# Kernel optimization log

Measured on AMD Instinct MI355X. Metric: run time of the kernel, lower is better.

Reference implementation:

```python
import jax, jax.numpy as jnp
import numpy as np

C_M, C_Z, C, N_HEAD = 256, 128, 32, 8
N_SEQ, N_RES = 256, 256
LN_EPS = 1e-5


def _layer_norm(x, w, b):
    mu = jnp.mean(x, axis=-1, keepdims=True)
    var = jnp.var(x, axis=-1, keepdims=True)
    return (x - mu) * jax.lax.rsqrt(var + LN_EPS) * w + b


def setup_inputs() -> dict:
    key = jax.random.key(0)
    ks = jax.random.split(key, 12)
    s = 0.02
    return {
        "m": jax.random.normal(ks[0], (N_SEQ, N_RES, C_M), dtype=jnp.float32),
        "z": jax.random.normal(ks[1], (N_RES, N_RES, C_Z), dtype=jnp.float32),
        "ln_m_w": jnp.ones((C_M,), jnp.float32),
        "ln_m_b": jnp.zeros((C_M,), jnp.float32),
        "ln_z_w": jnp.ones((C_Z,), jnp.float32),
        "ln_z_b": jnp.zeros((C_Z,), jnp.float32),
        "Wz": jax.random.normal(ks[2], (C_Z, N_HEAD), dtype=jnp.float32) * s,
        "Wq": jax.random.normal(ks[3], (C_M, N_HEAD * C), dtype=jnp.float32) * s,
        "Wk": jax.random.normal(ks[4], (C_M, N_HEAD * C), dtype=jnp.float32) * s,
        "Wv": jax.random.normal(ks[5], (C_M, N_HEAD * C), dtype=jnp.float32) * s,
        "Wg": jax.random.normal(ks[6], (C_M, N_HEAD * C), dtype=jnp.float32) * s,
        "bg": jnp.zeros((N_HEAD * C,), jnp.float32),
        "Wo": jax.random.normal(ks[7], (N_HEAD * C, C_M), dtype=jnp.float32) * s,
        "bo": jnp.zeros((C_M,), jnp.float32),
    }


def reference(m, z, ln_m_w, ln_m_b, ln_z_w, ln_z_b, Wz, Wq, Wk, Wv, Wg, bg, Wo, bo):
    S, R, cm = m.shape
    mn = _layer_norm(m, ln_m_w, ln_m_b)            # (S, R, c_m)
    zn = _layer_norm(z, ln_z_w, ln_z_b)            # (R, R, c_z)
    bias = jnp.einsum('qkz,zh->hqk', zn, Wz)       # (H, R, R), pair bias per head

    Wqh = Wq.reshape(cm, N_HEAD, C)
    Wkh = Wk.reshape(cm, N_HEAD, C)
    Wvh = Wv.reshape(cm, N_HEAD, C)
    q = jnp.einsum('srm,mhc->shrc', mn, Wqh)       # (S, H, R, c)
    k = jnp.einsum('srm,mhc->shrc', mn, Wkh)
    v = jnp.einsum('srm,mhc->shrc', mn, Wvh)

    scale = 1.0 / jnp.sqrt(jnp.asarray(C, mn.dtype))
    scores = jnp.einsum('shqc,shkc->shqk', q, k) * scale + bias[None]  # (S, H, R, R)
    attn = jax.nn.softmax(scores, axis=-1)
    o = jnp.einsum('shqk,shkc->shqc', attn, v)     # (S, H, R, c)
    o = o.transpose(0, 2, 1, 3).reshape(S, R, N_HEAD * C)

    g = jax.nn.sigmoid(mn @ Wg + bg)               # gating, (S, R, H*c)
    return (g * o) @ Wo + bo                       # (S, R, c_m)
```

## Files before the change

kernel.cpp:

```cpp
#include <hip/hip_runtime.h>
#include <cmath>

#define NSEQ 256
#define NRES 256
#define CM   256
#define CZ   128
#define NHEAD 8
#define CHD  32
#define NROW 65536

typedef __attribute__((ext_vector_type(8))) short short8;
typedef __attribute__((ext_vector_type(4))) short s16x4;
typedef __attribute__((ext_vector_type(4))) float f32x4;

__device__ __forceinline__ unsigned short f2bf(float x) {
    union { float f; unsigned int u; } v; v.f = x;
    unsigned int u = v.u;
    u += 0x7fffu + ((u >> 16) & 1u);
    return (unsigned short)(u >> 16);
}
__device__ __forceinline__ float bf2f(unsigned short b) {
    union { float f; unsigned int u; } v; v.u = ((unsigned int)b) << 16;
    return v.f;
}

__device__ __forceinline__ void async16(const void* g, void* l) {
    __builtin_amdgcn_global_load_lds(
        (const __attribute__((address_space(1))) unsigned int*)g,
        (__attribute__((address_space(3))) unsigned int*)l, 16, 0, 0);
}

__device__ __forceinline__ void xcd_remap(int& x, int& y) {
    const int nx = gridDim.x, ny = gridDim.y;
    const int b = blockIdx.x + blockIdx.y * nx;
    if ((ny & 7) == 0) {
        const int c = b & 7;
        const int t = b >> 3;
        x = t % nx;
        y = c + 8 * (t / nx);
    } else {
        x = blockIdx.x; y = blockIdx.y;
    }
}

__global__ void __launch_bounds__(64)
ln_m_kernel(const float* __restrict__ m, const float* __restrict__ w,
            const float* __restrict__ b, unsigned short* __restrict__ mbf) {
    const int row = blockIdx.x;
    const int t = threadIdx.x;
    const float* x = m + (size_t)row * CM;
    float4 xv = *(const float4*)(x + t * 4);
    float s  = xv.x + xv.y + xv.z + xv.w;
    float s2 = xv.x * xv.x + xv.y * xv.y + xv.z * xv.z + xv.w * xv.w;
#pragma unroll
    for (int off = 32; off > 0; off >>= 1) {
        s  += __shfl_xor(s, off);
        s2 += __shfl_xor(s2, off);
    }
    const float mu  = s * (1.0f / CM);
    const float var = s2 * (1.0f / CM) - mu * mu;
    const float inv = rsqrtf(var + 1e-5f);
    float4 wv = *(const float4*)(w + t * 4);
    float4 bv = *(const float4*)(b + t * 4);
    ushort4 o4;
    o4.x = f2bf((xv.x - mu) * inv * wv.x + bv.x);
    o4.y = f2bf((xv.y - mu) * inv * wv.y + bv.y);
    o4.z = f2bf((xv.z - mu) * inv * wv.z + bv.z);
    o4.w = f2bf((xv.w - mu) * inv * wv.w + bv.w);
    *(ushort4*)(mbf + (size_t)row * CM + t * 4) = o4;
}

__global__ void __launch_bounds__(64)
ln_z_bias_kernel(const float* __restrict__ z, const float* __restrict__ w,
                 const float* __restrict__ b, const float* __restrict__ Wz,
                 float* __restrict__ bias) {
    const int pair = blockIdx.x;
    const int t = threadIdx.x;
    const float* x = z + (size_t)pair * CZ;
    float2 xv = *(const float2*)(x + t * 2);
    float s  = xv.x + xv.y;
    float s2 = xv.x * xv.x + xv.y * xv.y;
#pragma unroll
    for (int off = 32; off > 0; off >>= 1) {
        s  += __shfl_xor(s, off);
        s2 += __shfl_xor(s2, off);
    }
    const float mu  = s * (1.0f / CZ);
    const float var = s2 * (1.0f / CZ) - mu * mu;
    const float inv = rsqrtf(var + 1e-5f);
    float2 wv = *(const float2*)(w + t * 2);
    float2 bv = *(const float2*)(b + t * 2);
    const float zn0 = (xv.x - mu) * inv * wv.x + bv.x;
    const float zn1 = (xv.y - mu) * inv * wv.y + bv.y;
    float ph[NHEAD];
#pragma unroll
    for (int h = 0; h < NHEAD; h++)
        ph[h] = zn0 * Wz[(2 * t) * NHEAD + h] + zn1 * Wz[(2 * t + 1) * NHEAD + h];
#pragma unroll
    for (int h = 0; h < NHEAD; h++) {
#pragma unroll
        for (int off = 32; off > 0; off >>= 1) ph[h] += __shfl_xor(ph[h], off);
    }
    if (t == 0) {
#pragma unroll
        for (int h = 0; h < NHEAD; h++)
            bias[(size_t)h * NROW + pair] = ph[h] * 1.4426950408889634f;
    }
}

__global__ void __launch_bounds__(256)
wsplit_kernel(const float* __restrict__ Wq, const float* __restrict__ Wk,
              const float* __restrict__ Wv, const float* __restrict__ Wg,
              const float* __restrict__ Wo, unsigned short* __restrict__ wbf) {
    const int n = blockIdx.x;
    const int mat = blockIdx.y;
    const int k = threadIdx.x;
    const float* W = (mat == 0) ? Wq : (mat == 1) ? Wk : (mat == 2) ? Wv
                   : (mat == 3) ? Wg : Wo;
    const float v = W[(size_t)k * 256 + n];
    unsigned short h = f2bf(v);
    unsigned short* hi = wbf + (size_t)mat * 65536;
    hi[(size_t)n * 256 + k] = h;
    if (mat == 4) {
        unsigned short* lo = wbf + (size_t)5 * 65536;
        lo[(size_t)n * 256 + k] = f2bf(v - bf2f(h));
    }
}

__device__ __forceinline__ void gemm128_1p(
    const unsigned short* __restrict__ A_g, const unsigned short* __restrict__ Bt_g,
    int m0, int n0, int rowsTot, short* A_s, short* B_s,
    unsigned short* __restrict__ C, const float* __restrict__ bias,
    float alpha, int act) {
    const int tid  = threadIdx.x;
    const int wid  = tid >> 6;
    const int lane = tid & 63;
    const int wm = (wid >> 1) * 64;
    const int wn = (wid & 1) * 64;

    f32x4 acc[4][4];
#pragma unroll
    for (int i = 0; i < 4; i++)
#pragma unroll
        for (int j = 0; j < 4; j++) acc[i][j] = (f32x4){0.f, 0.f, 0.f, 0.f};

    const unsigned short* gmat = (wid < 2) ? A_g : Bt_g;
    short* lmat = (wid < 2) ? A_s : B_s;
    const int brow = (wid < 2) ? m0 : n0;
    const int half = (wid & 1) * 64;
    const int srow = lane >> 2;
    const int skq  = (lane & 3) * 8;

    const int lrow = lane & 15;
    const int lk   = (lane >> 4) * 8;

    for (int k0 = 0; k0 < 256; k0 += 32) {
#pragma unroll
        for (int r = 0; r < 4; r++) {
            const unsigned short* g = gmat + (size_t)(brow + half + r * 16 + srow) * 256 + k0 + skq;
            short* l = lmat + (half + r * 16) * 32;
            async16(g, l);
        }
        __syncthreads();

        short8 ah[4], bh[4];
#pragma unroll
        for (int f = 0; f < 4; f++) {
            ah[f] = *(const short8*)&A_s[(wm + f * 16 + lrow) * 32 + lk];
            bh[f] = *(const short8*)&B_s[(wn + f * 16 + lrow) * 32 + lk];
        }
#pragma unroll
        for (int i = 0; i < 4; i++)
#pragma unroll
            for (int j = 0; j < 4; j++)
                acc[i][j] = __builtin_amdgcn_mfma_f32_16x16x32_bf16(ah[i], bh[j], acc[i][j], 0, 0, 0);
        __syncthreads();
    }

    const int ccol0 = lane & 15;
    const int crow0 = (lane >> 4) * 4;
    float bvv[4];
#pragma unroll
    for (int j = 0; j < 4; j++)
        bvv[j] = bias ? bias[n0 + wn + j * 16 + ccol0] : 0.0f;
#pragma unroll
    for (int i = 0; i < 4; i++) {
#pragma unroll
        for (int r = 0; r < 4; r++) {
            const int row = m0 + wm + i * 16 + crow0 + r;
#pragma unroll
            for (int j = 0; j < 4; j++) {
                const int col = n0 + wn + j * 16 + ccol0;
                float v = acc[i][j][r] * alpha + bvv[j];
                if (act == 1) v = 1.0f / (1.0f + __expf(-v));
                C[((size_t)(col >> 5) * rowsTot + row) * 32 + (col & 31)] = f2bf(v);
            }
        }
    }
}

__global__ void __launch_bounds__(256)
gemm_qkvg_kernel(const unsigned short* __restrict__ A,
                 const unsigned short* __restrict__ wbf,
                 unsigned short* __restrict__ qb, unsigned short* __restrict__ kb,
                 unsigned short* __restrict__ vb, unsigned short* __restrict__ gb,
                 const float* __restrict__ bg, float scale, int rowsTot) {
    __shared__ short A_s[128 * 32];
    __shared__ short B_s[128 * 32];
    int bx, by;
    xcd_remap(bx, by);
    const int which = bx >> 1;
    const int n0 = (bx & 1) * 128;
    const int m0 = by * 128;
    const unsigned short* bt = wbf + (size_t)which * 65536;
    unsigned short* C = (which == 0) ? qb : (which == 1) ? kb : (which == 2) ? vb : gb;
    const float alpha = (which == 0) ? scale : 1.0f;
    const float* bias = (which == 3) ? bg : nullptr;
    const int act = (which == 3) ? 1 : 0;
    gemm128_1p(A, bt, m0, n0, rowsTot, A_s, B_s, C, bias, alpha, act);
}

__global__ void __launch_bounds__(256)
gemm_out_kernel(const unsigned int* __restrict__ Ap_g,
                const unsigned short* __restrict__ wbf, float* __restrict__ C,
                const float* __restrict__ bo, int rowsTot) {
    __shared__ unsigned int Ap_s[128 * 32];
    __shared__ short Bhi_s[128 * 32];
    __shared__ short Blo_s[128 * 32];
    int bx, by;
    xcd_remap(bx, by);
    const int m0 = by * 128, n0 = bx * 128;
    const unsigned short* Bthi_g = wbf + (size_t)4 * 65536;
    const unsigned short* Btlo_g = wbf + (size_t)5 * 65536;

    const int tid  = threadIdx.x;
    const int wid  = tid >> 6;
    const int lane = tid & 63;
    const int wm = (wid >> 1) * 64;
    const int wn = (wid & 1) * 64;

    f32x4 acc[4][4];
#pragma unroll
    for (int i = 0; i < 4; i++)
#pragma unroll
        for (int j = 0; j < 4; j++) acc[i][j] = (f32x4){0.f, 0.f, 0.f, 0.f};

    const int lrow = lane & 15;
    const int lk   = (lane >> 4) * 8;

    for (int k0 = 0; k0 < 256; k0 += 32) {
        if (wid < 2) {
            const int half = wid * 64;
            const int srow = lane >> 3;
            const int scol = (lane & 7) * 4;
#pragma unroll
            for (int r = 0; r < 8; r++) {
                const unsigned int* g = Ap_g
                    + ((size_t)(k0 >> 5) * rowsTot + m0 + half + r * 8 + srow) * 32 + scol;
                unsigned int* l = Ap_s + (half + r * 8) * 32;
                async16(g, l);
            }
        } else {
            const unsigned short* gmat = (wid == 2) ? Bthi_g : Btlo_g;
            short* lmat = (wid == 2) ? Bhi_s : Blo_s;
            const int srow = lane >> 2;
            const int skq  = (lane & 3) * 8;
#pragma unroll
            for (int r = 0; r < 8; r++) {
                const unsigned short* g = gmat + (size_t)(n0 + r * 16 + srow) * 256 + k0 + skq;
                short* l = lmat + (r * 16) * 32;
                async16(g, l);
            }
        }
        __syncthreads();

        short8 ah[4], al[4], bh[4], bl[4];
#pragma unroll
        for (int f = 0; f < 4; f++) {
            const uint4* ap = (const uint4*)&Ap_s[(wm + f * 16 + lrow) * 32 + lk];
            uint4 a0 = ap[0], a1 = ap[1];
            union { unsigned int u[4]; short8 s; } uh, ul;
            uh.u[0] = __builtin_amdgcn_perm(a0.y, a0.x, 0x07060302u);
            uh.u[1] = __builtin_amdgcn_perm(a0.w, a0.z, 0x07060302u);
            uh.u[2] = __builtin_amdgcn_perm(a1.y, a1.x, 0x07060302u);
            uh.u[3] = __builtin_amdgcn_perm(a1.w, a1.z, 0x07060302u);
            ul.u[0] = __builtin_amdgcn_perm(a0.y, a0.x, 0x05040100u);
            ul.u[1] = __builtin_amdgcn_perm(a0.w, a0.z, 0x05040100u);
            ul.u[2] = __builtin_amdgcn_perm(a1.y, a1.x, 0x05040100u);
            ul.u[3] = __builtin_amdgcn_perm(a1.w, a1.z, 0x05040100u);
            ah[f] = uh.s; al[f] = ul.s;
            bh[f] = *(const short8*)&Bhi_s[(wn + f * 16 + lrow) * 32 + lk];
            bl[f] = *(const short8*)&Blo_s[(wn + f * 16 + lrow) * 32 + lk];
        }
#pragma unroll
        for (int i = 0; i < 4; i++)
#pragma unroll
            for (int j = 0; j < 4; j++) {
                acc[i][j] = __builtin_amdgcn_mfma_f32_16x16x32_bf16(ah[i], bh[j], acc[i][j], 0, 0, 0);
                acc[i][j] = __builtin_amdgcn_mfma_f32_16x16x32_bf16(ah[i], bl[j], acc[i][j], 0, 0, 0);
                acc[i][j] = __builtin_amdgcn_mfma_f32_16x16x32_bf16(al[i], bh[j], acc[i][j], 0, 0, 0);
            }
        __syncthreads();
    }

    const int ccol0 = lane & 15;
    const int crow0 = (lane >> 4) * 4;
    float bvv[4];
#pragma unroll
    for (int j = 0; j < 4; j++)
        bvv[j] = bo[n0 + wn + j * 16 + ccol0];
#pragma unroll
    for (int i = 0; i < 4; i++) {
#pragma unroll
        for (int r = 0; r < 4; r++) {
            const int row = m0 + wm + i * 16 + crow0 + r;
#pragma unroll
            for (int j = 0; j < 4; j++) {
                const int col = n0 + wn + j * 16 + ccol0;
                C[(size_t)row * 256 + col] = acc[i][j][r] + bvv[j];
            }
        }
    }
}

__global__ void __launch_bounds__(256, 4)
attn_mfma_kernel(const unsigned short* __restrict__ q, const unsigned short* __restrict__ k,
                 const unsigned short* __restrict__ v, const float* __restrict__ bias_qk,
                 const unsigned short* __restrict__ g,
                 unsigned int* __restrict__ opack, int rows) {
    const int s = blockIdx.x, h = blockIdx.y;
    __shared__ short Ks[256][40];
    __shared__ short Vs[32][268];
    __shared__ float li_s[4][64];
    const int tid = threadIdx.x;
    const int w = tid >> 6, l = tid & 63;
    const int lg = l >> 4, l15 = l & 15;
    const size_t hb = ((size_t)h * rows + (size_t)s * NRES) * 32;

    {
        const int kk0 = tid >> 2;
        const int c8 = (tid & 3) * 8;
#pragma unroll
        for (int r4 = 0; r4 < 4; r4++) {
            const int kk = r4 * 64 + kk0;
            const size_t gi = hb + (size_t)kk * 32 + c8;
            short8 k8 = *(const short8*)(k + gi);
            short8 v8 = *(const short8*)(v + gi);
            *(short8*)&Ks[kk][c8] = k8;
#pragma unroll
            for (int jj = 0; jj < 8; jj++) Vs[c8 + jj][kk] = v8[jj];
        }
    }
    const int wq0 = w * 64;
    short8 qf[4];
#pragma unroll
    for (int mq = 0; mq < 4; mq++)
        qf[mq] = *(const short8*)(q + hb + (size_t)(wq0 + mq * 16 + l15) * 32 + lg * 8);
    __syncthreads();

    f32x4 acco[4][2];
#pragma unroll
    for (int mq = 0; mq < 4; mq++)
#pragma unroll
        for (int nc = 0; nc < 2; nc++) acco[mq][nc] = (f32x4){0.f, 0.f, 0.f, 0.f};
    float lip[4] = {0.f, 0.f, 0.f, 0.f};
    const float* bh = bias_qk + (size_t)h * NROW;

    for (int ch = 0; ch < 8; ch++) {
        const int kb = ch * 32;
        short8 kf[2];
#pragma unroll
        for (int ik = 0; ik < 2; ik++)
            kf[ik] = *(const short8*)&Ks[kb + ik * 16 + l15][lg * 8];
#pragma unroll
        for (int ik = 0; ik < 2; ik++) {
            s16x4 vf[2];
#pragma unroll
            for (int nc = 0; nc < 2; nc++)
                vf[nc] = *(const s16x4*)&Vs[nc * 16 + l15][kb + ik * 16 + lg * 4];
            const int kkr = ik * 16 + lg * 4;
#pragma unroll
            for (int jq = 0; jq < 4; jq++) {
                const int qrow = wq0 + jq * 16 + l15;
                f32x4 sa = (f32x4){0.f, 0.f, 0.f, 0.f};
                sa = __builtin_amdgcn_mfma_f32_16x16x32_bf16(kf[ik], qf[jq], sa, 0, 0, 0);
                float4 bv = *(const float4*)(bh + (size_t)qrow * NRES + kb + kkr);
                const float p0 = __builtin_amdgcn_exp2f(sa[0] + bv.x);
                const float p1 = __builtin_amdgcn_exp2f(sa[1] + bv.y);
                const float p2 = __builtin_amdgcn_exp2f(sa[2] + bv.z);
                const float p3 = __builtin_amdgcn_exp2f(sa[3] + bv.w);
                lip[jq] += (p0 + p1) + (p2 + p3);
                s16x4 pa;
                pa[0] = (short)f2bf(p0); pa[1] = (short)f2bf(p1);
                pa[2] = (short)f2bf(p2); pa[3] = (short)f2bf(p3);
#pragma unroll
                for (int nc = 0; nc < 2; nc++)
                    acco[jq][nc] = __builtin_amdgcn_mfma_f32_16x16x16bf16_1k(
                        pa, vf[nc], acco[jq][nc], 0, 0, 0);
            }
        }
    }

#pragma unroll
    for (int jq = 0; jq < 4; jq++) {
        lip[jq] += __shfl_xor(lip[jq], 16);
        lip[jq] += __shfl_xor(lip[jq], 32);
        li_s[w][jq * 16 + l15] = lip[jq];
    }

#pragma unroll
    for (int mq = 0; mq < 4; mq++) {
#pragma unroll
        for (int r = 0; r < 4; r++) {
            const int qrow = wq0 + mq * 16 + lg * 4 + r;
            const float inv = 1.0f / li_s[w][mq * 16 + lg * 4 + r];
            const size_t rb = hb + (size_t)qrow * 32;
#pragma unroll
            for (int nc = 0; nc < 2; nc++) {
                const int c = nc * 16 + l15;
                const float val = acco[mq][nc][r] * inv * bf2f(g[rb + c]);
                const unsigned short hi = f2bf(val);
                const unsigned short lo = f2bf(val - bf2f(hi));
                opack[rb + c] = ((unsigned int)hi << 16) | lo;
            }
        }
    }
}

extern "C" void kernel_launch(void* const* d_in, const int* in_sizes, int n_in,
                              void* d_out, int out_size, void* d_ws, size_t ws_size,
                              hipStream_t stream) {
    const float* m    = (const float*)d_in[0];
    const float* z    = (const float*)d_in[1];
    const float* lnmw = (const float*)d_in[2];
    const float* lnmb = (const float*)d_in[3];
    const float* lnzw = (const float*)d_in[4];
    const float* lnzb = (const float*)d_in[5];
    const float* Wz   = (const float*)d_in[6];
    const float* Wq   = (const float*)d_in[7];
    const float* Wk   = (const float*)d_in[8];
    const float* Wv   = (const float*)d_in[9];
    const float* Wg   = (const float*)d_in[10];
    const float* bg   = (const float*)d_in[11];
    const float* Wo   = (const float*)d_in[12];
    const float* bo   = (const float*)d_in[13];
    float* out = (float*)d_out;

    char* wsb = (char*)d_ws;
    const size_t BIASB = (size_t)NHEAD * NROW * 4;
    const size_t WBFB  = (size_t)6 * 65536 * 2;
    float* bias_qk = (float*)wsb;
    unsigned short* wbf = (unsigned short*)(wsb + BIASB);
    char* chunk0 = wsb + BIASB + ((WBFB + 255) & ~(size_t)255);

    const size_t avail = ws_size - (size_t)(chunk0 - wsb);
    int SC = NSEQ;
    while (SC > 1 && (size_t)SC * NRES * CM * 14 > avail) SC >>= 1;
    const size_t CHE = (size_t)SC * NRES * CM;

    unsigned short* qb  = (unsigned short*)chunk0;
    unsigned short* kb  = qb + CHE;
    unsigned short* vb  = kb + CHE;
    unsigned short* gb  = vb + CHE;
    unsigned short* mbf = gb + CHE;
    unsigned int* opk   = (unsigned int*)(mbf + CHE);

    ln_z_bias_kernel<<<NROW, 64, 0, stream>>>(z, lnzw, lnzb, Wz, bias_qk);
    wsplit_kernel<<<dim3(256, 5), 256, 0, stream>>>(Wq, Wk, Wv, Wg, Wo, wbf);

    const int rows = SC * NRES;
    const int mtiles = rows / 128;
    const float scale = 0.17677669529663687f * 1.4426950408889634f;

    for (int s0 = 0; s0 < NSEQ; s0 += SC) {
        const float* m_c   = m   + (size_t)s0 * NRES * CM;
        float*       out_c = out + (size_t)s0 * NRES * CM;

        ln_m_kernel<<<rows, 64, 0, stream>>>(m_c, lnmw, lnmb, mbf);

        gemm_qkvg_kernel<<<dim3(8, mtiles), 256, 0, stream>>>(
            mbf, wbf, qb, kb, vb, gb, bg, scale, rows);

        attn_mfma_kernel<<<dim3(SC, NHEAD), 256, 0, stream>>>(
            qb, kb, vb, bias_qk, gb, opk, rows);

        gemm_out_kernel<<<dim3(2, mtiles), 256, 0, stream>>>(
            opk, wbf, out_c, bo, rows);
    }
}
```

Measured before the change: 373.1 us.

## Widen QKVG GEMM K-step to 64 with XOR-swizzled LDS and staged stores

The QKVG projection GEMM is inlined into its kernel and now loads K tiles of 64 instead of 32, which halves the number of barrier-separated iterations. The LDS layout uses an XOR swizzle on 16-byte slots to avoid bank conflicts when fragments are read. The epilogue writes results into LDS first, then emits coalesced 16-byte stores to the head-planar output instead of scattered 2-byte stores. LDS use per block grows to 32KB, which may limit occupancy.

```diff
diff --git a/kernel.cpp b/kernel.cpp
--- a/kernel.cpp
+++ b/kernel.cpp
@@ -127,97 +127,109 @@
     }
 }
 
-__device__ __forceinline__ void gemm128_1p(
-    const unsigned short* __restrict__ A_g, const unsigned short* __restrict__ Bt_g,
-    int m0, int n0, int rowsTot, short* A_s, short* B_s,
-    unsigned short* __restrict__ C, const float* __restrict__ bias,
-    float alpha, int act) {
-    const int tid  = threadIdx.x;
-    const int wid  = tid >> 6;
-    const int lane = tid & 63;
-    const int wm = (wid >> 1) * 64;
-    const int wn = (wid & 1) * 64;
-
-    f32x4 acc[4][4];
-#pragma unroll
-    for (int i = 0; i < 4; i++)
-#pragma unroll
-        for (int j = 0; j < 4; j++) acc[i][j] = (f32x4){0.f, 0.f, 0.f, 0.f};
-
-    const unsigned short* gmat = (wid < 2) ? A_g : Bt_g;
-    short* lmat = (wid < 2) ? A_s : B_s;
-    const int brow = (wid < 2) ? m0 : n0;
-    const int half = (wid & 1) * 64;
-    const int srow = lane >> 2;
-    const int skq  = (lane & 3) * 8;
-
-    const int lrow = lane & 15;
-    const int lk   = (lane >> 4) * 8;
-
-    for (int k0 = 0; k0 < 256; k0 += 32) {
-#pragma unroll
-        for (int r = 0; r < 4; r++) {
-            const unsigned short* g = gmat + (size_t)(brow + half + r * 16 + srow) * 256 + k0 + skq;
-            short* l = lmat + (half + r * 16) * 32;
-            async16(g, l);
-        }
-        __syncthreads();
-
-        short8 ah[4], bh[4];
-#pragma unroll
-        for (int f = 0; f < 4; f++) {
-            ah[f] = *(const short8*)&A_s[(wm + f * 16 + lrow) * 32 + lk];
-            bh[f] = *(const short8*)&B_s[(wn + f * 16 + lrow) * 32 + lk];
-        }
-#pragma unroll
-        for (int i = 0; i < 4; i++)
-#pragma unroll
-            for (int j = 0; j < 4; j++)
-                acc[i][j] = __builtin_amdgcn_mfma_f32_16x16x32_bf16(ah[i], bh[j], acc[i][j], 0, 0, 0);
-        __syncthreads();
-    }
-
-    const int ccol0 = lane & 15;
-    const int crow0 = (lane >> 4) * 4;
-    float bvv[4];
-#pragma unroll
-    for (int j = 0; j < 4; j++)
-        bvv[j] = bias ? bias[n0 + wn + j * 16 + ccol0] : 0.0f;
-#pragma unroll
-    for (int i = 0; i < 4; i++) {
-#pragma unroll
-        for (int r = 0; r < 4; r++) {
-            const int row = m0 + wm + i * 16 + crow0 + r;
-#pragma unroll
-            for (int j = 0; j < 4; j++) {
-                const int col = n0 + wn + j * 16 + ccol0;
-                float v = acc[i][j][r] * alpha + bvv[j];
-                if (act == 1) v = 1.0f / (1.0f + __expf(-v));
-                C[((size_t)(col >> 5) * rowsTot + row) * 32 + (col & 31)] = f2bf(v);
-            }
-        }
-    }
-}
-
 __global__ void __launch_bounds__(256)
 gemm_qkvg_kernel(const unsigned short* __restrict__ A,
                  const unsigned short* __restrict__ wbf,
                  unsigned short* __restrict__ qb, unsigned short* __restrict__ kb,
                  unsigned short* __restrict__ vb, unsigned short* __restrict__ gb,
                  const float* __restrict__ bg, float scale, int rowsTot) {
-    __shared__ short A_s[128 * 32];
-    __shared__ short B_s[128 * 32];
+    __shared__ short LDS[128 * 128];
+    short* A_s = LDS;
+    short* B_s = LDS + 128 * 64;
     int bx, by;
     xcd_remap(bx, by);
     const int which = bx >> 1;
     const int n0 = (bx & 1) * 128;
     const int m0 = by * 128;
-    const unsigned short* bt = wbf + (size_t)which * 65536;
+    const unsigned short* Bt_g = wbf + (size_t)which * 65536;
     unsigned short* C = (which == 0) ? qb : (which == 1) ? kb : (which == 2) ? vb : gb;
     const float alpha = (which == 0) ? scale : 1.0f;
     const float* bias = (which == 3) ? bg : nullptr;
     const int act = (which == 3) ? 1 : 0;
-    gemm128_1p(A, bt, m0, n0, rowsTot, A_s, B_s, C, bias, alpha, act);
+
+    const int tid  = threadIdx.x;
+    const int wid  = tid >> 6;
+    const int lane = tid & 63;
+    const int wm = (wid >> 1) * 64;
+    const int wn = (wid & 1) * 64;
+
+    f32x4 acc[4][4];
+#pragma unroll
+    for (int i = 0; i < 4; i++)
+#pragma unroll
+        for (int j = 0; j < 4; j++) acc[i][j] = (f32x4){0.f, 0.f, 0.f, 0.f};
+
+    const unsigned short* gmat = (wid < 2) ? A : Bt_g;
+    short* lmat = (wid < 2) ? A_s : B_s;
+    const int brow = (wid < 2) ? m0 : n0;
+    const int half = (wid & 1) * 64;
+    const int srow  = lane >> 3;
+    const int sslot = (lane & 7) ^ srow;
+
+    const int lrow = lane & 15;
+    const int lg   = lane >> 4;
+    const int x0 = ((0 + lg) ^ (lane & 7)) * 8;
+    const int x1 = ((4 + lg) ^ (lane & 7)) * 8;
+
+    for (int k0 = 0; k0 < 256; k0 += 64) {
+#pragma unroll
+        for (int r = 0; r < 8; r++) {
+            const unsigned short* g = gmat
+                + (size_t)(brow + half + r * 8 + srow) * 256 + k0 + sslot * 8;
+            short* l = lmat + (half + r * 8) * 64;
+            async16(g, l);
+        }
+        __syncthreads();
+
+#pragma unroll
+        for (int kk = 0; kk < 2; kk++) {
+            const int x = kk ? x1 : x0;
+            short8 af[4], bf[4];
+#pragma unroll
+            for (int f = 0; f < 4; f++) {
+                af[f] = *(const short8*)&A_s[(wm + f * 16 + lrow) * 64 + x];
+                bf[f] = *(const short8*)&B_s[(wn + f * 16 + lrow) * 64 + x];
+            }
+#pragma unroll
+            for (int i = 0; i < 4; i++)
+#pragma unroll
+                for (int j = 0; j < 4; j++)
+                    acc[i][j] = __builtin_amdgcn_mfma_f32_16x16x32_bf16(af[i], bf[j], acc[i][j], 0, 0, 0);
+        }
+        __syncthreads();
+    }
+
+    {
+        const int ccol0 = lane & 15;
+        const int crow0 = lg * 4;
+        float bvv[4];
+#pragma unroll
+        for (int j = 0; j < 4; j++)
+            bvv[j] = bias ? bias[n0 + wn + j * 16 + ccol0] : 0.0f;
+#pragma unroll
+        for (int i = 0; i < 4; i++)
+#pragma unroll
+            for (int r = 0; r < 4; r++) {
+                const int row = wm + i * 16 + crow0 + r;
+#pragma unroll
+                for (int j = 0; j < 4; j++) {
+                    float vv = acc[i][j][r] * alpha + bvv[j];
+                    if (act == 1) vv = 1.0f / (1.0f + __expf(-vv));
+                    LDS[row * 128 + wn + j * 16 + ccol0] = (short)f2bf(vv);
+                }
+            }
+        __syncthreads();
+        const int rr = tid >> 4;
+        const int cb = (tid & 15) * 8;
+        const int pl = n0 / 32 + (cb >> 5);
+        const int cw = cb & 31;
+#pragma unroll
+        for (int t = 0; t < 8; t++) {
+            const int row = t * 16 + rr;
+            short8 vv = *(const short8*)&LDS[row * 128 + cb];
+            *(short8*)&C[((size_t)pl * rowsTot + m0 + row) * 32 + cw] = vv;
+        }
+    }
 }
 
 __global__ void __launch_bounds__(256)
```

New measurement: 370.0 us. Within noise of the previous version (-0.8%).
